# Optimization experiments

Hardware: AMD Instinct MI355X
Metric: run time of the kernel (lower is better)

## Reference

```python
import jax, jax.numpy as jnp
import numpy as np

EPS = 1e-5

def _ln(v, gamma, beta):
    mu = jnp.mean(v, axis=-1, keepdims=True)
    var = jnp.mean(jnp.square(v - mu), axis=-1, keepdims=True)
    return (v - mu) * jax.lax.rsqrt(var + EPS) * gamma + beta

def setup_inputs() -> dict:
    B, T, D = 8, 2048, 2048
    NG = 3  # n_strands - 1
    key = jax.random.key(0)
    ks = jax.random.split(key, 8)
    s = lambda k, shp, fan: jax.random.normal(k, shp, jnp.float32) * (1.0 / np.sqrt(fan))
    return {
        "x": jax.random.normal(ks[0], (B, T, D), jnp.float32),
        "W1": s(ks[1], (D, 2 * D), 2 * D), "b1": jnp.zeros((D,), jnp.float32),
        "W2": s(ks[2], (2 * NG, D), D), "b2": jnp.zeros((2 * NG,), jnp.float32),
        "Wp": s(ks[3], (D, D), D), "bp": jnp.zeros((D,), jnp.float32),
        "gamma": jnp.ones((D,), jnp.float32), "beta": jnp.zeros((D,), jnp.float32),
    }

def reference(x, W1, b1, W2, b2, Wp, bp, gamma, beta):
    # Adjacent-pair crossing features: pair_t = [x_t, x_{t+1}], t = 0..T-2
    pair = jnp.concatenate([x[:, :-1], x[:, 1:]], axis=-1)          # (B,T-1,2D)
    h = jax.nn.gelu(jnp.einsum('btk,dk->btd', pair, W1) + b1, approximate=False)
    logits = jnp.einsum('btd,gd->btg', h, W2) + b2                   # (B,T-1,2*NG)
    scale = jnp.mean(jax.nn.softmax(logits, axis=-1), axis=-1, keepdims=True)  # (B,T-1,1)
    P = jnp.einsum('btd,ed->bte', x, Wp) + bp                        # mix_proj(x)
    m = P[:, 1:] * scale    # added to position t at step t
    mp = P[:, :-1] * scale  # added to position t+1 at step t
    # Loop semantics: pos t first updated as j at step t-1, then as i at step t.
    tmp = jnp.concatenate([x[:, :1], _ln(x[:, 1:] + mp, gamma, beta)], axis=1)
    out = jnp.concatenate([_ln(tmp[:, :-1] + m, gamma, beta), tmp[:, -1:]], axis=1)
    return out
```

## Files before the change

### kernel.cpp

```cpp
#include <hip/hip_runtime.h>
#include <hip/hip_bf16.h>
#include <stdint.h>


#define B_DIM 8
#define T_DIM 2048
#define D_DIM 2048
#define M_DIM (B_DIM * T_DIM)
#define N_DIM D_DIM
#define K_DIM D_DIM

typedef __attribute__((ext_vector_type(8))) short short8;
typedef __attribute__((ext_vector_type(4))) float f32x4;

__device__ inline unsigned short f2bf(float f) {
    unsigned u = __float_as_uint(f);
    u += 0x7fffu + ((u >> 16) & 1u);
    return (unsigned short)(u >> 16);
}
__device__ inline float bf2f(unsigned u16) {
    return __uint_as_float(u16 << 16);
}
__device__ inline void unpack8(uint4 u, float* f) {
    f[0] = bf2f(u.x & 0xffffu); f[1] = bf2f(u.x >> 16);
    f[2] = bf2f(u.y & 0xffffu); f[3] = bf2f(u.y >> 16);
    f[4] = bf2f(u.z & 0xffffu); f[5] = bf2f(u.z >> 16);
    f[6] = bf2f(u.w & 0xffffu); f[7] = bf2f(u.w >> 16);
}

__device__ inline void async_ld16(const void* g, void* l) {
    __builtin_amdgcn_global_load_lds(
        (__attribute__((address_space(1))) void*)(g),
        (__attribute__((address_space(3))) void*)(l),
        16, 0, 0);
}

__global__ void cast_f32_bf16(const float* __restrict__ x, unsigned short* __restrict__ Xb,
                              const float* __restrict__ Wp, unsigned short* __restrict__ Wb,
                              int nx4, int ntot4) {
    int i = blockIdx.x * blockDim.x + threadIdx.x;
    if (i >= ntot4) return;
    const float* src; unsigned short* dst; int j;
    if (i < nx4) { src = x; dst = Xb; j = i; }
    else         { src = Wp; dst = Wb; j = i - nx4; }
    float4 f = ((const float4*)src)[j];
    ushort4 o;
    o.x = f2bf(f.x); o.y = f2bf(f.y); o.z = f2bf(f.z); o.w = f2bf(f.w);
    ((ushort4*)dst)[j] = o;
}

__global__ void gemm_bt(const unsigned short* __restrict__ Xb,
                        const unsigned short* __restrict__ Wb,
                        const float* __restrict__ bp,
                        unsigned short* __restrict__ P)
{
    __shared__ unsigned short As[128 * 64];
    __shared__ unsigned short Bs[128 * 64];

    const int tid  = threadIdx.x;
    const int lane = tid & 63;
    const int wave = tid >> 6;
    const int m0 = blockIdx.y * 128;
    const int n0 = blockIdx.x * 128;

    const int rw = (wave >> 1) * 64;
    const int cw = (wave & 1) * 64;
    const int fr = lane & 15;
    const int lq = lane >> 4;

    int s_r[4], s_l[4], s_ci[4];
#pragma unroll
    for (int q = 0; q < 4; q++) {
        int ci = (wave * 4 + q) * 64 + lane;
        s_ci[q] = ci;
        s_r[q] = ci >> 3;
        s_l[q] = (ci & 7) ^ (s_r[q] & 7);
    }

    f32x4 acc[4][4];
#pragma unroll
    for (int i = 0; i < 4; i++)
#pragma unroll
        for (int j = 0; j < 4; j++) acc[i][j] = (f32x4){0.f, 0.f, 0.f, 0.f};

    for (int k0 = 0; k0 < K_DIM; k0 += 64) {
#pragma unroll
        for (int q = 0; q < 4; q++) {
            async_ld16(Xb + (size_t)(m0 + s_r[q]) * K_DIM + k0 + s_l[q] * 8,
                       As + s_ci[q] * 8);
            async_ld16(Wb + (size_t)(n0 + s_r[q]) * K_DIM + k0 + s_l[q] * 8,
                       Bs + s_ci[q] * 8);
        }
        __syncthreads();

#pragma unroll
        for (int kk = 0; kk < 2; kk++) {
            const int l = kk * 4 + lq;
            short8 a[4], b[4];
#pragma unroll
            for (int i = 0; i < 4; i++) {
                int row = rw + 16 * i + fr;
                a[i] = *(const short8*)(As + row * 64 + (l ^ (row & 7)) * 8);
            }
#pragma unroll
            for (int j = 0; j < 4; j++) {
                int row = cw + 16 * j + fr;
                b[j] = *(const short8*)(Bs + row * 64 + (l ^ (row & 7)) * 8);
            }
#pragma unroll
            for (int i = 0; i < 4; i++)
#pragma unroll
                for (int j = 0; j < 4; j++)
                    acc[i][j] = __builtin_amdgcn_mfma_f32_16x16x32_bf16(a[i], b[j], acc[i][j], 0, 0, 0);
        }
        __syncthreads();
    }

    const int crow = (lane >> 4) * 4;
    const int ccol = lane & 15;
#pragma unroll
    for (int j = 0; j < 4; j++) {
        int col = n0 + cw + 16 * j + ccol;
        float bpv = bp[col];
#pragma unroll
        for (int i = 0; i < 4; i++) {
            size_t base = (size_t)(m0 + rw + 16 * i + crow) * N_DIM + col;
#pragma unroll
            for (int r = 0; r < 4; r++)
                P[base + (size_t)r * N_DIM] = f2bf(acc[i][j][r] + bpv);
        }
    }
}

__device__ inline void ln_stage(float* v, const float* g, const float* be, float* sm, int tid) {
    float s = 0.f, q = 0.f;
#pragma unroll
    for (int i = 0; i < 8; i++) { s += v[i]; q += v[i] * v[i]; }
#pragma unroll
    for (int off = 32; off; off >>= 1) { s += __shfl_down(s, off); q += __shfl_down(q, off); }
    int w = tid >> 6;
    if ((tid & 63) == 0) { sm[w * 2] = s; sm[w * 2 + 1] = q; }
    __syncthreads();
    s = sm[0] + sm[2] + sm[4] + sm[6];
    q = sm[1] + sm[3] + sm[5] + sm[7];
    __syncthreads();
    const float invD = 1.0f / (float)D_DIM;
    float mu = s * invD;
    float var = q * invD - mu * mu;
    float rs = rsqrtf(var + 1e-5f);
#pragma unroll
    for (int i = 0; i < 8; i++) v[i] = (v[i] - mu) * rs * g[i] + be[i];
}

__global__ void ln_kernel(const unsigned short* __restrict__ Xb,
                          const unsigned short* __restrict__ P,
                          const float* __restrict__ gamma,
                          const float* __restrict__ beta,
                          float* __restrict__ out)
{
    const int r = blockIdx.x;
    const int t = r & (T_DIM - 1);
    const int tid = threadIdx.x;
    __shared__ float sm[8];

    float v[8], g[8], be[8];
    unpack8(((const uint4*)(Xb + (size_t)r * D_DIM))[tid], v);
    {
        float4 g0 = ((const float4*)gamma)[2 * tid], g1 = ((const float4*)gamma)[2 * tid + 1];
        g[0] = g0.x; g[1] = g0.y; g[2] = g0.z; g[3] = g0.w;
        g[4] = g1.x; g[5] = g1.y; g[6] = g1.z; g[7] = g1.w;
        float4 b0 = ((const float4*)beta)[2 * tid], b1 = ((const float4*)beta)[2 * tid + 1];
        be[0] = b0.x; be[1] = b0.y; be[2] = b0.z; be[3] = b0.w;
        be[4] = b1.x; be[5] = b1.y; be[6] = b1.z; be[7] = b1.w;
    }

    const float inv6 = 1.0f / 6.0f;

    if (t > 0) {
        float p[8];
        unpack8(((const uint4*)(P + (size_t)(r - 1) * D_DIM))[tid], p);
#pragma unroll
        for (int i = 0; i < 8; i++) v[i] += p[i] * inv6;
        ln_stage(v, g, be, sm, tid);
    }
    if (t < T_DIM - 1) {
        float p[8];
        unpack8(((const uint4*)(P + (size_t)(r + 1) * D_DIM))[tid], p);
#pragma unroll
        for (int i = 0; i < 8; i++) v[i] += p[i] * inv6;
        ln_stage(v, g, be, sm, tid);
    }

    float4* orow = (float4*)(out + (size_t)r * D_DIM);
    orow[2 * tid]     = (float4){v[0], v[1], v[2], v[3]};
    orow[2 * tid + 1] = (float4){v[4], v[5], v[6], v[7]};
}

extern "C" void kernel_launch(void* const* d_in, const int* in_sizes, int n_in,
                              void* d_out, int out_size, void* d_ws, size_t ws_size,
                              hipStream_t stream) {
    const float* x     = (const float*)d_in[0];
    const float* Wp    = (const float*)d_in[5];
    const float* bp    = (const float*)d_in[6];
    const float* gamma = (const float*)d_in[7];
    const float* beta  = (const float*)d_in[8];
    float* out = (float*)d_out;

    unsigned short* Xb = (unsigned short*)d_ws;
    unsigned short* Wb = Xb + (size_t)M_DIM * K_DIM;
    unsigned short* P  = Wb + (size_t)N_DIM * K_DIM;

    const int nx4   = (M_DIM * K_DIM) / 4;
    const int ntot4 = nx4 + (N_DIM * K_DIM) / 4;
    cast_f32_bf16<<<(ntot4 + 255) / 256, 256, 0, stream>>>(x, Xb, Wp, Wb, nx4, ntot4);

    dim3 ggrid(N_DIM / 128, M_DIM / 128);
    gemm_bt<<<ggrid, 256, 0, stream>>>(Xb, Wb, bp, P);
    ln_kernel<<<M_DIM, 256, 0, stream>>>(Xb, P, gamma, beta, out);
}
```

Measured before the change: 421.1 us.

## Rewrite GEMM as double-buffered 256x256 pipelined kernel and use wave-per-row LayerNorm

Result: no change. 423.4 us (+0.5%).

```diff
diff --git a/kernel.cpp b/kernel.cpp
--- a/kernel.cpp
+++ b/kernel.cpp
@@ -1,5 +1,4 @@
 #include <hip/hip_runtime.h>
-#include <hip/hip_bf16.h>
 #include <stdint.h>
 
 
@@ -9,6 +8,7 @@
 #define M_DIM (B_DIM * T_DIM)
 #define N_DIM D_DIM
 #define K_DIM D_DIM
+#define NT (K_DIM / 64)
 
 typedef __attribute__((ext_vector_type(8))) short short8;
 typedef __attribute__((ext_vector_type(4))) float f32x4;
@@ -27,13 +27,15 @@
     f[4] = bf2f(u.z & 0xffffu); f[5] = bf2f(u.z >> 16);
     f[6] = bf2f(u.w & 0xffffu); f[7] = bf2f(u.w >> 16);
 }
-
 __device__ inline void async_ld16(const void* g, void* l) {
     __builtin_amdgcn_global_load_lds(
         (__attribute__((address_space(1))) void*)(g),
         (__attribute__((address_space(3))) void*)(l),
         16, 0, 0);
 }
+
+#define VMCNT(n) asm volatile("s_waitcnt vmcnt(" #n ")" ::: "memory")
+#define LGKM0    asm volatile("s_waitcnt lgkmcnt(0)" ::: "memory")
 
 __global__ void cast_f32_bf16(const float* __restrict__ x, unsigned short* __restrict__ Xb,
                               const float* __restrict__ Wp, unsigned short* __restrict__ Wb,
@@ -49,151 +51,264 @@
     ((ushort4*)dst)[j] = o;
 }
 
-__global__ void gemm_bt(const unsigned short* __restrict__ Xb,
-                        const unsigned short* __restrict__ Wb,
-                        const float* __restrict__ bp,
-                        unsigned short* __restrict__ P)
+
+template <int PP>
+__device__ __attribute__((always_inline)) inline
+void mfma16(f32x4 (&acc)[8][4], const short8 (&a)[2][2], const short8 (&b)[4][2]) {
+#pragma unroll
+    for (int kk = 0; kk < 2; ++kk)
+#pragma unroll
+        for (int i = 0; i < 2; ++i)
+#pragma unroll
+            for (int j = 0; j < 4; ++j)
+                acc[PP * 2 + i][j] = __builtin_amdgcn_mfma_f32_16x16x32_bf16(
+                    a[i][kk], b[j][kk], acc[PP * 2 + i][j], 0, 0, 0);
+}
+
+__global__ __launch_bounds__(512, 2)
+void gemm_bt(const unsigned short* __restrict__ Xb,
+             const unsigned short* __restrict__ Wb,
+             const float* __restrict__ bp,
+             unsigned short* __restrict__ P)
 {
-    __shared__ unsigned short As[128 * 64];
-    __shared__ unsigned short Bs[128 * 64];
+    __shared__ unsigned short As[2][256 * 64];
+    __shared__ unsigned short Bs[2][256 * 64];
 
     const int tid  = threadIdx.x;
     const int lane = tid & 63;
     const int wave = tid >> 6;
-    const int m0 = blockIdx.y * 128;
-    const int n0 = blockIdx.x * 128;
-
-    const int rw = (wave >> 1) * 64;
-    const int cw = (wave & 1) * 64;
+    const int wm = wave >> 2;
+    const int wn = wave & 3;
     const int fr = lane & 15;
     const int lq = lane >> 4;
-
-    int s_r[4], s_l[4], s_ci[4];
-#pragma unroll
-    for (int q = 0; q < 4; q++) {
-        int ci = (wave * 4 + q) * 64 + lane;
-        s_ci[q] = ci;
-        s_r[q] = ci >> 3;
-        s_l[q] = (ci & 7) ^ (s_r[q] & 7);
-    }
-
-    f32x4 acc[4][4];
-#pragma unroll
-    for (int i = 0; i < 4; i++)
-#pragma unroll
-        for (int j = 0; j < 4; j++) acc[i][j] = (f32x4){0.f, 0.f, 0.f, 0.f};
-
-    for (int k0 = 0; k0 < K_DIM; k0 += 64) {
-#pragma unroll
-        for (int q = 0; q < 4; q++) {
-            async_ld16(Xb + (size_t)(m0 + s_r[q]) * K_DIM + k0 + s_l[q] * 8,
-                       As + s_ci[q] * 8);
-            async_ld16(Wb + (size_t)(n0 + s_r[q]) * K_DIM + k0 + s_l[q] * 8,
-                       Bs + s_ci[q] * 8);
-        }
-        __syncthreads();
-
-#pragma unroll
-        for (int kk = 0; kk < 2; kk++) {
-            const int l = kk * 4 + lq;
-            short8 a[4], b[4];
-#pragma unroll
-            for (int i = 0; i < 4; i++) {
-                int row = rw + 16 * i + fr;
-                a[i] = *(const short8*)(As + row * 64 + (l ^ (row & 7)) * 8);
-            }
-#pragma unroll
-            for (int j = 0; j < 4; j++) {
-                int row = cw + 16 * j + fr;
-                b[j] = *(const short8*)(Bs + row * 64 + (l ^ (row & 7)) * 8);
-            }
-#pragma unroll
-            for (int i = 0; i < 4; i++)
-#pragma unroll
-                for (int j = 0; j < 4; j++)
-                    acc[i][j] = __builtin_amdgcn_mfma_f32_16x16x32_bf16(a[i], b[j], acc[i][j], 0, 0, 0);
-        }
-        __syncthreads();
+    const int xa = fr & 7;
+
+    const int bid = blockIdx.x;
+    const int swz = (bid & 7) * 64 + (bid >> 3);
+    const int m0 = (swz >> 3) * 256;
+    const int n0 = (swz & 7) * 256;
+
+    const int rr = tid >> 3;
+    const int cc = tid & 7;
+    const int lc8 = (cc ^ (rr & 7)) * 8;
+    const unsigned short* Ag = Xb + (size_t)(m0 + rr) * K_DIM + lc8;
+    const unsigned short* Bg = Wb + (size_t)(n0 + rr) * K_DIM + lc8;
+
+#define STAGE_A(buf, g, k0) async_ld16(Ag + (size_t)(g) * 64 * K_DIM + (k0), \
+                                       &As[buf][((g) * 64 + rr) * 64 + cc * 8])
+#define STAGE_B(buf, g, k0) async_ld16(Bg + (size_t)(g) * 64 * K_DIM + (k0), \
+                                       &Bs[buf][((g) * 64 + rr) * 64 + cc * 8])
+#define LDA(dst, buf, p, i, kk) dst = *(const short8*)&As[buf][ \
+        (wm * 128 + (p) * 32 + (i) * 16 + fr) * 64 + ((((kk) * 4 + lq) ^ xa) * 8)]
+#define LDB(dst, buf, j, kk)    dst = *(const short8*)&Bs[buf][ \
+        (wn * 64 + (j) * 16 + fr) * 64 + ((((kk) * 4 + lq) ^ xa) * 8)]
+
+    f32x4 acc[8][4];
+#pragma unroll
+    for (int i = 0; i < 8; ++i)
+#pragma unroll
+        for (int j = 0; j < 4; ++j) acc[i][j] = (f32x4){0.f, 0.f, 0.f, 0.f};
+
+    STAGE_B(0, 0, 0); STAGE_B(0, 1, 0); STAGE_B(0, 2, 0); STAGE_B(0, 3, 0);
+    STAGE_A(0, 0, 0); STAGE_A(0, 2, 0); STAGE_A(0, 1, 0); STAGE_A(0, 3, 0);
+    VMCNT(2);
+    __builtin_amdgcn_s_barrier();
+
+    short8 a[2][2], b[4][2];
+    for (int t = 0; t < NT - 1; ++t) {
+        const int cur = t & 1, nxt = cur ^ 1;
+        const int kn = (t + 1) * 64;
+
+        LDB(b[0][0], cur, 0, 0); LDB(b[0][1], cur, 0, 1);
+        LDB(b[1][0], cur, 1, 0); LDB(b[1][1], cur, 1, 1);
+        LDB(b[2][0], cur, 2, 0); LDB(b[2][1], cur, 2, 1);
+        LDB(b[3][0], cur, 3, 0); LDB(b[3][1], cur, 3, 1);
+        LDA(a[0][0], cur, 0, 0, 0); LDA(a[0][1], cur, 0, 0, 1);
+        LDA(a[1][0], cur, 0, 1, 0); LDA(a[1][1], cur, 0, 1, 1);
+        STAGE_B(nxt, 0, kn); STAGE_B(nxt, 1, kn);
+        __builtin_amdgcn_s_barrier();
+        LGKM0; __builtin_amdgcn_sched_barrier(0);
+        __builtin_amdgcn_s_setprio(1);
+        mfma16<0>(acc, a, b);
+        __builtin_amdgcn_s_setprio(0);
+        __builtin_amdgcn_s_barrier();
+
+        LDA(a[0][0], cur, 1, 0, 0); LDA(a[0][1], cur, 1, 0, 1);
+        LDA(a[1][0], cur, 1, 1, 0); LDA(a[1][1], cur, 1, 1, 1);
+        STAGE_B(nxt, 2, kn); STAGE_B(nxt, 3, kn);
+        __builtin_amdgcn_s_barrier();
+        LGKM0; __builtin_amdgcn_sched_barrier(0);
+        __builtin_amdgcn_s_setprio(1);
+        mfma16<1>(acc, a, b);
+        __builtin_amdgcn_s_setprio(0);
+        VMCNT(4);
+        __builtin_amdgcn_s_barrier();
+
+        LDA(a[0][0], cur, 2, 0, 0); LDA(a[0][1], cur, 2, 0, 1);
+        LDA(a[1][0], cur, 2, 1, 0); LDA(a[1][1], cur, 2, 1, 1);
+        STAGE_A(nxt, 0, kn); STAGE_A(nxt, 2, kn);
+        __builtin_amdgcn_s_barrier();
+        LGKM0; __builtin_amdgcn_sched_barrier(0);
+        __builtin_amdgcn_s_setprio(1);
+        mfma16<2>(acc, a, b);
+        __builtin_amdgcn_s_setprio(0);
+        __builtin_amdgcn_s_barrier();
+
+        LDA(a[0][0], cur, 3, 0, 0); LDA(a[0][1], cur, 3, 0, 1);
+        LDA(a[1][0], cur, 3, 1, 0); LDA(a[1][1], cur, 3, 1, 1);
+        STAGE_A(nxt, 1, kn); STAGE_A(nxt, 3, kn);
+        __builtin_amdgcn_s_barrier();
+        LGKM0; __builtin_amdgcn_sched_barrier(0);
+        __builtin_amdgcn_s_setprio(1);
+        mfma16<3>(acc, a, b);
+        __builtin_amdgcn_s_setprio(0);
+        VMCNT(2);
+        __builtin_amdgcn_s_barrier();
+    }
+
+    {
+        const int cur = (NT - 1) & 1;
+        LDB(b[0][0], cur, 0, 0); LDB(b[0][1], cur, 0, 1);
+        LDB(b[1][0], cur, 1, 0); LDB(b[1][1], cur, 1, 1);
+        LDB(b[2][0], cur, 2, 0); LDB(b[2][1], cur, 2, 1);
+        LDB(b[3][0], cur, 3, 0); LDB(b[3][1], cur, 3, 1);
+        LDA(a[0][0], cur, 0, 0, 0); LDA(a[0][1], cur, 0, 0, 1);
+        LDA(a[1][0], cur, 0, 1, 0); LDA(a[1][1], cur, 0, 1, 1);
+        __builtin_amdgcn_s_barrier();
+        LGKM0; __builtin_amdgcn_sched_barrier(0);
+        __builtin_amdgcn_s_setprio(1);
+        mfma16<0>(acc, a, b);
+        __builtin_amdgcn_s_setprio(0);
+        __builtin_amdgcn_s_barrier();
+
+        LDA(a[0][0], cur, 1, 0, 0); LDA(a[0][1], cur, 1, 0, 1);
+        LDA(a[1][0], cur, 1, 1, 0); LDA(a[1][1], cur, 1, 1, 1);
+        __builtin_amdgcn_s_barrier();
+        LGKM0; __builtin_amdgcn_sched_barrier(0);
+        __builtin_amdgcn_s_setprio(1);
+        mfma16<1>(acc, a, b);
+        __builtin_amdgcn_s_setprio(0);
+        VMCNT(0);
+        __builtin_amdgcn_s_barrier();
+
+        LDA(a[0][0], cur, 2, 0, 0); LDA(a[0][1], cur, 2, 0, 1);
+        LDA(a[1][0], cur, 2, 1, 0); LDA(a[1][1], cur, 2, 1, 1);
+        __builtin_amdgcn_s_barrier();
+        LGKM0; __builtin_amdgcn_sched_barrier(0);
+        __builtin_amdgcn_s_setprio(1);
+        mfma16<2>(acc, a, b);
+        __builtin_amdgcn_s_setprio(0);
+        __builtin_amdgcn_s_barrier();
+
+        LDA(a[0][0], cur, 3, 0, 0); LDA(a[0][1], cur, 3, 0, 1);
+        LDA(a[1][0], cur, 3, 1, 0); LDA(a[1][1], cur, 3, 1, 1);
+        LGKM0; __builtin_amdgcn_sched_barrier(0);
+        __builtin_amdgcn_s_setprio(1);
+        mfma16<3>(acc, a, b);
+        __builtin_amdgcn_s_setprio(0);
     }
 
     const int crow = (lane >> 4) * 4;
     const int ccol = lane & 15;
 #pragma unroll
-    for (int j = 0; j < 4; j++) {
-        int col = n0 + cw + 16 * j + ccol;
-        float bpv = bp[col];
-#pragma unroll
-        for (int i = 0; i < 4; i++) {
-            size_t base = (size_t)(m0 + rw + 16 * i + crow) * N_DIM + col;
-#pragma unroll
-            for (int r = 0; r < 4; r++)
-                P[base + (size_t)r * N_DIM] = f2bf(acc[i][j][r] + bpv);
+    for (int j = 0; j < 4; ++j) {
+        const int col = n0 + wn * 64 + 16 * j + ccol;
+        const float bpv = bp[col];
+#pragma unroll
+        for (int mi = 0; mi < 8; ++mi) {
+            size_t base = (size_t)(m0 + wm * 128 + 16 * mi + crow) * N_DIM + col;
+#pragma unroll
+            for (int r = 0; r < 4; ++r)
+                P[base + (size_t)r * N_DIM] = f2bf(acc[mi][j][r] + bpv);
         }
     }
-}
-
-__device__ inline void ln_stage(float* v, const float* g, const float* be, float* sm, int tid) {
+#undef STAGE_A
+#undef STAGE_B
+#undef LDA
+#undef LDB
+}
+
+__device__ __attribute__((always_inline)) inline
+void ln_wave(float* v, const float* __restrict__ gamma, const float* __restrict__ beta,
+             int lane) {
     float s = 0.f, q = 0.f;
 #pragma unroll
-    for (int i = 0; i < 8; i++) { s += v[i]; q += v[i] * v[i]; }
-#pragma unroll
-    for (int off = 32; off; off >>= 1) { s += __shfl_down(s, off); q += __shfl_down(q, off); }
-    int w = tid >> 6;
-    if ((tid & 63) == 0) { sm[w * 2] = s; sm[w * 2 + 1] = q; }
-    __syncthreads();
-    s = sm[0] + sm[2] + sm[4] + sm[6];
-    q = sm[1] + sm[3] + sm[5] + sm[7];
-    __syncthreads();
+    for (int i = 0; i < 32; ++i) { s += v[i]; q += v[i] * v[i]; }
+#pragma unroll
+    for (int off = 32; off; off >>= 1) {
+        s += __shfl_xor(s, off);
+        q += __shfl_xor(q, off);
+    }
     const float invD = 1.0f / (float)D_DIM;
-    float mu = s * invD;
-    float var = q * invD - mu * mu;
-    float rs = rsqrtf(var + 1e-5f);
-#pragma unroll
-    for (int i = 0; i < 8; i++) v[i] = (v[i] - mu) * rs * g[i] + be[i];
-}
-
-__global__ void ln_kernel(const unsigned short* __restrict__ Xb,
-                          const unsigned short* __restrict__ P,
-                          const float* __restrict__ gamma,
-                          const float* __restrict__ beta,
-                          float* __restrict__ out)
+    const float mu = s * invD;
+    const float rs = rsqrtf(q * invD - mu * mu + 1e-5f);
+    const float4* g4 = (const float4*)gamma;
+    const float4* b4 = (const float4*)beta;
+#pragma unroll
+    for (int c = 0; c < 4; ++c) {
+        const int e = (c * 64 + lane) * 2;
+        float4 g0 = g4[e], g1 = g4[e + 1];
+        float4 b0 = b4[e], b1 = b4[e + 1];
+        v[c*8+0] = (v[c*8+0] - mu) * rs * g0.x + b0.x;
+        v[c*8+1] = (v[c*8+1] - mu) * rs * g0.y + b0.y;
+        v[c*8+2] = (v[c*8+2] - mu) * rs * g0.z + b0.z;
+        v[c*8+3] = (v[c*8+3] - mu) * rs * g0.w + b0.w;
+        v[c*8+4] = (v[c*8+4] - mu) * rs * g1.x + b1.x;
+        v[c*8+5] = (v[c*8+5] - mu) * rs * g1.y + b1.y;
+        v[c*8+6] = (v[c*8+6] - mu) * rs * g1.z + b1.z;
+        v[c*8+7] = (v[c*8+7] - mu) * rs * g1.w + b1.w;
+    }
+}
+
+__global__ __launch_bounds__(256)
+void ln_kernel(const unsigned short* __restrict__ Xb,
+               const unsigned short* __restrict__ P,
+               const float* __restrict__ gamma,
+               const float* __restrict__ beta,
+               float* __restrict__ out)
 {
-    const int r = blockIdx.x;
+    const int lane = threadIdx.x & 63;
+    const int r = blockIdx.x * 4 + (threadIdx.x >> 6);
     const int t = r & (T_DIM - 1);
-    const int tid = threadIdx.x;
-    __shared__ float sm[8];
-
-    float v[8], g[8], be[8];
-    unpack8(((const uint4*)(Xb + (size_t)r * D_DIM))[tid], v);
-    {
-        float4 g0 = ((const float4*)gamma)[2 * tid], g1 = ((const float4*)gamma)[2 * tid + 1];
-        g[0] = g0.x; g[1] = g0.y; g[2] = g0.z; g[3] = g0.w;
-        g[4] = g1.x; g[5] = g1.y; g[6] = g1.z; g[7] = g1.w;
-        float4 b0 = ((const float4*)beta)[2 * tid], b1 = ((const float4*)beta)[2 * tid + 1];
-        be[0] = b0.x; be[1] = b0.y; be[2] = b0.z; be[3] = b0.w;
-        be[4] = b1.x; be[5] = b1.y; be[6] = b1.z; be[7] = b1.w;
-    }
-
     const float inv6 = 1.0f / 6.0f;
 
+    float v[32];
+    const uint4* xrow = (const uint4*)(Xb + (size_t)r * D_DIM);
+#pragma unroll
+    for (int c = 0; c < 4; ++c) {
+        float f[8]; unpack8(xrow[c * 64 + lane], f);
+#pragma unroll
+        for (int jj = 0; jj < 8; ++jj) v[c * 8 + jj] = f[jj];
+    }
+
     if (t > 0) {
-        float p[8];
-        unpack8(((const uint4*)(P + (size_t)(r - 1) * D_DIM))[tid], p);
-#pragma unroll
-        for (int i = 0; i < 8; i++) v[i] += p[i] * inv6;
-        ln_stage(v, g, be, sm, tid);
+        const uint4* prow = (const uint4*)(P + (size_t)(r - 1) * D_DIM);
+#pragma unroll
+        for (int c = 0; c < 4; ++c) {
+            float f[8]; unpack8(prow[c * 64 + lane], f);
+#pragma unroll
+            for (int jj = 0; jj < 8; ++jj) v[c * 8 + jj] += f[jj] * inv6;
+        }
+        ln_wave(v, gamma, beta, lane);
     }
     if (t < T_DIM - 1) {
-        float p[8];
-        unpack8(((const uint4*)(P + (size_t)(r + 1) * D_DIM))[tid], p);
-#pragma unroll
-        for (int i = 0; i < 8; i++) v[i] += p[i] * inv6;
-        ln_stage(v, g, be, sm, tid);
+        const uint4* prow = (const uint4*)(P + (size_t)(r + 1) * D_DIM);
+#pragma unroll
+        for (int c = 0; c < 4; ++c) {
+            float f[8]; unpack8(prow[c * 64 + lane], f);
+#pragma unroll
+            for (int jj = 0; jj < 8; ++jj) v[c * 8 + jj] += f[jj] * inv6;
+        }
+        ln_wave(v, gamma, beta, lane);
     }
 
     float4* orow = (float4*)(out + (size_t)r * D_DIM);
-    orow[2 * tid]     = (float4){v[0], v[1], v[2], v[3]};
-    orow[2 * tid + 1] = (float4){v[4], v[5], v[6], v[7]};
+#pragma unroll
+    for (int c = 0; c < 4; ++c) {
+        const int e = (c * 64 + lane) * 2;
+        orow[e]     = (float4){v[c*8+0], v[c*8+1], v[c*8+2], v[c*8+3]};
+        orow[e + 1] = (float4){v[c*8+4], v[c*8+5], v[c*8+6], v[c*8+7]};
+    }
 }
 
 extern "C" void kernel_launch(void* const* d_in, const int* in_sizes, int n_in,
@@ -214,7 +329,6 @@
     const int ntot4 = nx4 + (N_DIM * K_DIM) / 4;
     cast_f32_bf16<<<(ntot4 + 255) / 256, 256, 0, stream>>>(x, Xb, Wp, Wb, nx4, ntot4);
 
-    dim3 ggrid(N_DIM / 128, M_DIM / 128);
-    gemm_bt<<<ggrid, 256, 0, stream>>>(Xb, Wb, bp, P);
-    ln_kernel<<<M_DIM, 256, 0, stream>>>(Xb, P, gamma, beta, out);
-}
+    gemm_bt<<<(M_DIM / 256) * (N_DIM / 256), 512, 0, stream>>>(Xb, Wb, bp, P);
+    ln_kernel<<<M_DIM / 4, 256, 0, stream>>>(Xb, P, gamma, beta, out);
+}
```
